# Kernel optimization log

Hardware: AMD Instinct MI355X
Metric: run time of the kernel (lower is better)

The kernel has to match this reference:

```python
import jax, jax.numpy as jnp
import numpy as np

M, N, P, T = 8000, 63, 64, 5


def setup_inputs() -> dict:
    key = jax.random.key(0)
    ks = jax.random.split(key, 19)
    sn = (1.0 / N) ** 0.5
    sp = (1.0 / P) ** 0.5
    f32 = jnp.float32
    return {
        "A": jax.random.normal(ks[0], (1, M, N), f32),
        "b": jax.random.normal(ks[1], (1, M), f32),
        "c": jax.random.normal(ks[2], (1, N), f32),
        "theta1r": sn * jax.random.normal(ks[3], (P, N + 1), f32),
        "theta1c": sn * jax.random.normal(ks[4], (P, N + 1), f32),
        "theta2rr": sp * jax.random.normal(ks[5], (P, P), f32),
        "theta2rc": sp * jax.random.normal(ks[6], (P, P), f32),
        "theta2cr": sp * jax.random.normal(ks[7], (P, P), f32),
        "theta3rr": sp * jax.random.normal(ks[8], (P, P), f32),
        "theta3rc": sp * jax.random.normal(ks[9], (P, P), f32),
        "theta3cr": sp * jax.random.normal(ks[10], (P, P), f32),
        "theta4rr": sp * jax.random.normal(ks[11], (P,), f32),
        "theta4rc": sp * jax.random.normal(ks[12], (P,), f32),
        "theta4cr": sp * jax.random.normal(ks[13], (P,), f32),
        "theta6r": sp * jax.random.normal(ks[14], (P, P), f32),
        "theta6c": sp * jax.random.normal(ks[15], (P, P), f32),
        "theta7": sp * jax.random.normal(ks[16], (P, P), f32),
        "W8": 0.05 * jax.random.normal(ks[17], (2, 2 * P), f32),
        "b8": 0.05 * jax.random.normal(ks[18], (2,), f32),
        "z": 7,
    }


def reference(A, b, c, theta1r, theta1c, theta2rr, theta2rc, theta2cr,
              theta3rr, theta3rc, theta3cr, theta4rr, theta4rc, theta4cr,
              theta6r, theta6c, theta7, W8, b8, z):
    relu = jax.nn.relu
    m, n = A.shape[1], A.shape[2]
    p = theta1r.shape[0]
    # raw node features: row node v -> [A[v,:], b[v]]; column node m -> [c, 0]
    Fr_raw = jnp.concatenate([A[0], b[0][:, None]], axis=1)        # (m, n+1)
    fc_raw = jnp.concatenate([c[0], jnp.zeros((1,), A.dtype)])     # (n+1,)
    Fr = Fr_raw / jnp.linalg.norm(Fr_raw, axis=1, keepdims=True)   # f(v), v < m
    fc = fc_raw / jnp.linalg.norm(fc_raw)                          # f(m)
    # edge weights w(v,u) = f(v).f(u) are detached in the original (float(...data))
    Frd = jax.lax.stop_gradient(Fr)
    fcd = jax.lax.stop_gradient(fc)
    Wrr = Frd @ Frd.T                                              # (m, m)
    dg = jnp.diagonal(Wrr)
    srr_pos = relu(Wrr).sum(axis=1) - relu(dg)                     # sum over u != v
    srr_neg = relu(-Wrr).sum(axis=1) - relu(-dg)
    wrc = Frd @ fcd                                                # (m,) = w(v, m)
    # identity: sum_u relu(t4 * w_u) = relu(t4) * sum_u relu(w_u) + relu(-t4) * sum_u relu(-w_u)
    Srr = relu(theta4rr)[:, None] * srr_pos[None, :] + relu(-theta4rr)[:, None] * srr_neg[None, :]
    Src = relu(theta4rc)[:, None] * relu(wrc)[None, :] + relu(-theta4rc)[:, None] * relu(-wrc)[None, :]
    scr = relu(theta4cr) * relu(wrc).sum() + relu(-theta4cr) * relu(-wrc).sum()
    edge_r = theta3rr @ Srr + theta3rc @ Src                       # (p, m), constant over t
    edge_c = theta3cr @ scr                                        # (p,)
    fz = Fr[z]                                                     # z < m: row node feature
    t1r = theta1r @ fz                                             # (p,)
    t1c = theta1c @ fz
    # mu init (p, m+1) = [[Ab^T, c0^T]; 0]; split into row columns / column node
    mu_r0 = jnp.zeros((p, m), A.dtype).at[: n + 1].set(Fr_raw.T)
    mu_c0 = jnp.zeros((p,), A.dtype).at[: n + 1].set(fc_raw)

    def step(carry, _):
        mu_r, mu_c = carry
        # row nodes: term2rr uses old mu[:, v]; term2rc uses old mu[:, m]
        new_r = relu(t1r[:, None] + theta2rr @ mu_r + (theta2rc @ mu_c)[:, None] + edge_r)
        # column node updated last within a sweep -> sees updated row embeddings
        new_c = relu(t1c + theta2cr @ new_r.sum(axis=1) + edge_c)
        return (new_r, new_c), None

    (mu_r, mu_c), _ = jax.lax.scan(step, (mu_r0, mu_c0), None, length=T)
    term6 = theta6r @ mu_r.sum(axis=1) + theta6c @ mu_c            # (p,)
    term7 = theta7 @ mu_r[:, z]                                    # (p,)
    feat = jax.nn.sigmoid(jnp.concatenate([term6, term7]))         # (2p,)
    return (feat @ W8.T + b8)[None, :]                             # (1, 2)
```

## Files before the change

kernel.cpp:

```cpp
#include <hip/hip_runtime.h>
#include <math.h>

typedef __attribute__((ext_vector_type(8))) short short8;
typedef __attribute__((ext_vector_type(4))) float f32x4;

#define WS_SPART 0
#define WS_GPART 262144
#define WS_WPART 270336
#define WS_CPART 270592
#define WS_T1R   310592
#define WS_T1C   310656
#define WS_AL    310720
#define WS_BE    310784
#define WS_GA    310848
#define WS_DE    310912
#define WS_ECP   310976
#define WS_ECN   311040
#define WS_W     311104
#define WS_MUZ   311168
#define WS_WSUM  311232
#define WS_RNORM 311296
#define WS_R2H   319488
#define WS_R2L   321536
#define WS_E4    323584
#define WS_FH    355584
#define WS_FL    617728

__device__ __forceinline__ float waveReduceSum(float v) {
#pragma unroll
    for (int m = 32; m >= 1; m >>= 1) v += __shfl_xor(v, m, 64);
    return v;
}
__device__ __forceinline__ unsigned short f2bf(float f) {
    unsigned int u = __float_as_uint(f);
    unsigned int r = (u + 0x7fffu + ((u >> 16) & 1u)) >> 16;
    return (unsigned short)r;
}
__device__ __forceinline__ float bf2f(unsigned short h) {
    return __uint_as_float(((unsigned int)h) << 16);
}

__global__ __launch_bounds__(256) void k_fr(
    const float* __restrict__ A, const float* __restrict__ b, const float* __restrict__ c,
    const float* __restrict__ th1r, const float* __restrict__ th1c,
    const float* __restrict__ th2rr, const float* __restrict__ th2rc,
    const float* __restrict__ th3rr, const float* __restrict__ th3rc, const float* __restrict__ th3cr,
    const float* __restrict__ th4rr, const float* __restrict__ th4rc, const float* __restrict__ th4cr,
    const int* __restrict__ zp,
    unsigned short* __restrict__ Fh, unsigned short* __restrict__ Fl,
    unsigned short* __restrict__ R2H, unsigned short* __restrict__ R2L,
    float* __restrict__ ws)
{
    int tid = threadIdx.x, lane = tid & 63, wid = tid >> 6;

    if (blockIdx.x == 128) {
        __shared__ float fcraw[64], fz[64], sh4a[64], sh4b[64];
        int p = lane;
        int z = zp[0];
        float cv = (p < 63) ? c[p] : 0.f;
        fcraw[p] = cv;
        float av = (p < 63) ? A[z * 63 + p] : b[z];
        float s2 = waveReduceSum(av * av);
        fz[p] = av * rsqrtf(s2);
        __syncthreads();

        float t1 = 0.f, t2 = 0.f, w0 = 0.f;
#pragma unroll 8
        for (int k = 0; k < 64; k++) {
            t1 += th1r[p * 64 + k] * fz[k];
            t2 += th1c[p * 64 + k] * fz[k];
            w0 += th2rc[p * 64 + k] * fcraw[k];
        }
        ws[WS_T1R + p] = t1;
        ws[WS_T1C + p] = t2;
        ws[WS_W + p] = t1 + w0;

        sh4a[p] = th4rr[p];
        sh4b[p] = th4rc[p];
        __syncthreads();
        float a = 0.f, bb = 0.f, g = 0.f, d = 0.f;
#pragma unroll 8
        for (int k = 0; k < 64; k++) {
            float t4 = sh4a[k];
            a  += th3rr[p * 64 + k] * fmaxf(t4, 0.f);
            bb += th3rr[p * 64 + k] * fmaxf(-t4, 0.f);
            float t5 = sh4b[k];
            g  += th3rc[p * 64 + k] * fmaxf(t5, 0.f);
            d  += th3rc[p * 64 + k] * fmaxf(-t5, 0.f);
        }
        ws[WS_AL + p] = a; ws[WS_BE + p] = bb;
        ws[WS_GA + p] = g; ws[WS_DE + p] = d;
        __syncthreads();
        sh4a[p] = th4cr[p];
        __syncthreads();
        float e1 = 0.f, e2 = 0.f;
#pragma unroll 8
        for (int k = 0; k < 64; k++) {
            float t6 = sh4a[k];
            e1 += th3cr[p * 64 + k] * fmaxf(t6, 0.f);
            e2 += th3cr[p * 64 + k] * fmaxf(-t6, 0.f);
        }
        ws[WS_ECP + p] = e1; ws[WS_ECN + p] = e2;

#pragma unroll
        for (int i = 0; i < 16; i++) {
            int idx = tid * 16 + i;
            float f = th2rr[idx];
            unsigned short h = f2bf(f);
            R2H[idx] = h;
            R2L[idx] = f2bf(f - bf2f(h));
        }
        return;
    }

    __shared__ float gsh[64];
    __shared__ float wsh2[2];
    if (tid < 64) gsh[tid] = 0.f;
    if (tid < 2) wsh2[tid] = 0.f;
    __syncthreads();

    float cv = (lane < 63) ? c[lane] : 0.f;
    float cn2 = waveReduceSum(cv * cv);
    float fcnl = cv * rsqrtf(cn2);

    int gw = blockIdx.x * 4 + wid;
    float gl = 0.f, lp = 0.f, ln = 0.f;
    for (int r = gw; r < 8192; r += 512) {
        if (r < 8000) {
            float val = (lane < 63) ? A[r * 63 + lane] : b[r];
            float s2 = waveReduceSum(val * val);
            float f = val * rsqrtf(s2);
            unsigned short h = f2bf(f);
            Fh[r * 64 + lane] = h;
            Fl[r * 64 + lane] = f2bf(f - bf2f(h));
            gl += f;
            float w = waveReduceSum(f * fcnl);
            if (lane == 0) {
                ws[WS_RNORM + r] = sqrtf(s2);
                lp += fmaxf(w, 0.f); ln += fmaxf(-w, 0.f);
            }
        } else {
            Fh[r * 64 + lane] = 0;
            Fl[r * 64 + lane] = 0;
        }
    }
    atomicAdd(&gsh[lane], gl);
    if (lane == 0) { atomicAdd(&wsh2[0], lp); atomicAdd(&wsh2[1], ln); }
    __syncthreads();
    if (tid < 64) ws[WS_GPART + blockIdx.x * 64 + tid] = gsh[tid];
    if (tid == 64) ws[WS_WPART + blockIdx.x * 2 + 0] = wsh2[0];
    if (tid == 65) ws[WS_WPART + blockIdx.x * 2 + 1] = wsh2[1];
}

__global__ __launch_bounds__(256) void k_gram(
    const unsigned short* __restrict__ Fh, const unsigned short* __restrict__ Fl,
    float* __restrict__ ws)
{
    int tid = threadIdx.x, lane = tid & 63, wid = tid >> 6;
    int m = lane & 15, quad = lane >> 4;
    int vbase = blockIdx.x * 256 + wid * 64;

    short8 AH[8], AL[8];
#pragma unroll
    for (int pt = 0; pt < 4; pt++)
#pragma unroll
        for (int q = 0; q < 2; q++) {
            int off = (vbase + pt * 16 + m) * 64 + q * 32 + quad * 8;
            AH[pt * 2 + q] = *(const short8*)(Fh + off);
            AL[pt * 2 + q] = *(const short8*)(Fl + off);
        }
    float srr[16];
#pragma unroll
    for (int i = 0; i < 16; i++) srr[i] = 0.f;

    const int y = blockIdx.y;
    const int boff = m * 64 + quad * 8;
    short8 B0h[2], B0l[2], B1h[2], B1l[2];
#pragma unroll
    for (int q = 0; q < 2; q++) {
        B0h[q] = *(const short8*)(Fh + y * 16 * 64 + boff + q * 32);
        B0l[q] = *(const short8*)(Fl + y * 16 * 64 + boff + q * 32);
    }
#pragma unroll 1
    for (int ii = 0; ii < 8; ii++) {
        int tB1 = y + 64 * ii + 32;
#pragma unroll
        for (int q = 0; q < 2; q++) {
            B1h[q] = *(const short8*)(Fh + tB1 * 16 * 64 + boff + q * 32);
            B1l[q] = *(const short8*)(Fl + tB1 * 16 * 64 + boff + q * 32);
        }
#pragma unroll
        for (int pt = 0; pt < 4; pt++) {
            f32x4 a = {0.f, 0.f, 0.f, 0.f};
#pragma unroll
            for (int q = 0; q < 2; q++) {
                a = __builtin_amdgcn_mfma_f32_16x16x32_bf16(AH[pt*2+q], B0h[q], a, 0, 0, 0);
                a = __builtin_amdgcn_mfma_f32_16x16x32_bf16(AH[pt*2+q], B0l[q], a, 0, 0, 0);
                a = __builtin_amdgcn_mfma_f32_16x16x32_bf16(AL[pt*2+q], B0h[q], a, 0, 0, 0);
            }
#pragma unroll
            for (int r = 0; r < 4; r++) srr[pt*4+r] += fmaxf(a[r], 0.f);
        }
        if (ii < 7) {
            int tB0 = y + 64 * ii + 64;
#pragma unroll
            for (int q = 0; q < 2; q++) {
                B0h[q] = *(const short8*)(Fh + tB0 * 16 * 64 + boff + q * 32);
                B0l[q] = *(const short8*)(Fl + tB0 * 16 * 64 + boff + q * 32);
            }
        }
#pragma unroll
        for (int pt = 0; pt < 4; pt++) {
            f32x4 a = {0.f, 0.f, 0.f, 0.f};
#pragma unroll
            for (int q = 0; q < 2; q++) {
                a = __builtin_amdgcn_mfma_f32_16x16x32_bf16(AH[pt*2+q], B1h[q], a, 0, 0, 0);
                a = __builtin_amdgcn_mfma_f32_16x16x32_bf16(AH[pt*2+q], B1l[q], a, 0, 0, 0);
                a = __builtin_amdgcn_mfma_f32_16x16x32_bf16(AL[pt*2+q], B1h[q], a, 0, 0, 0);
            }
#pragma unroll
            for (int r = 0; r < 4; r++) srr[pt*4+r] += fmaxf(a[r], 0.f);
        }
    }
#pragma unroll
    for (int pt = 0; pt < 4; pt++)
#pragma unroll
        for (int r = 0; r < 4; r++) {
            float s = srr[pt * 4 + r];
#pragma unroll
            for (int mm = 8; mm >= 1; mm >>= 1) s += __shfl_xor(s, mm, 64);
            if (m == 0)
                ws[WS_SPART + y * 8192 + vbase + pt * 16 + quad * 4 + r] = s;
        }
}

__global__ __launch_bounds__(256) void k_e4(
    const float* __restrict__ c, float* __restrict__ ws,
    unsigned short* __restrict__ MH, unsigned short* __restrict__ ML)
{
    __shared__ float fcnS[64], gS[64], sprow[64], red[256];
    int tid = threadIdx.x, lane = tid & 63, wid = tid >> 6;

    float cv = (lane < 63) ? c[lane] : 0.f;
    float cn2 = waveReduceSum(cv * cv);
    if (wid == 0) fcnS[lane] = cv * rsqrtf(cn2);

    float gv = 0.f;
#pragma unroll 8
    for (int blk = wid * 32; blk < wid * 32 + 32; blk++)
        gv += ws[WS_GPART + blk * 64 + lane];
    red[tid] = gv;
    __syncthreads();
    if (tid < 64) gS[tid] = red[tid] + red[64 + tid] + red[128 + tid] + red[192 + tid];
    if (wid == 1) {
        float wp = ws[WS_WPART + lane * 2] + ws[WS_WPART + (lane + 64) * 2];
        wp = waveReduceSum(wp);
        if (lane == 0) ws[WS_WSUM] = wp;
    }
    if (wid == 2) {
        float wn = ws[WS_WPART + lane * 2 + 1] + ws[WS_WPART + (lane + 64) * 2 + 1];
        wn = waveReduceSum(wn);
        if (lane == 0) ws[WS_WSUM + 1] = wn;
    }
    int v0 = blockIdx.x * 64;
    float sv = 0.f;
#pragma unroll
    for (int y = wid * 8; y < wid * 8 + 8; y++)
        sv += ws[WS_SPART + y * 8192 + v0 + lane];
    __syncthreads();
    red[tid] = sv;
    __syncthreads();
    if (tid < 64) sprow[tid] = red[tid] + red[64 + tid] + red[128 + tid] + red[192 + tid];
    __syncthreads();

    for (int i2 = 0; i2 < 16; i2++) {
        int i = wid * 16 + i2;
        int v = v0 + i;
        unsigned short fh = MH[v * 64 + lane];
        unsigned short fl = ML[v * 64 + lane];
        float fr = bf2f(fh) + bf2f(fl);
        float dw = waveReduceSum(fr * fcnS[lane]);
        float dg = waveReduceSum(fr * gS[lane]);
        if (lane == 0) {
            float spv = sprow[i];
            float4 e;
            e.x = spv - 1.0f;
            e.y = spv - dg;
            e.z = fmaxf(dw, 0.f);
            e.w = fmaxf(-dw, 0.f);
            *(float4*)(ws + WS_E4 + v * 4) = e;
        }
        float rnv = ws[WS_RNORM + v];
        float x = fr * rnv;
        unsigned short h = f2bf(x);
        MH[v * 64 + lane] = h;
        ML[v * 64 + lane] = f2bf(x - bf2f(h));
    }
}

__global__ __launch_bounds__(256) void k_iter(
    const float* __restrict__ th2cr, const float* __restrict__ th2rc,
    const int* __restrict__ zp, float* __restrict__ ws,
    unsigned short* __restrict__ MH, unsigned short* __restrict__ ML,
    const unsigned short* __restrict__ R2H, const unsigned short* __restrict__ R2L,
    int t)
{
    __shared__ __align__(16) float wsh[64], alS[64], beS[64], gaS[64], deS[64];
    __shared__ float red[256], Ssh[64], ysh[64], colp[256];
    int tid = threadIdx.x, lane = tid & 63, wid = tid >> 6;
    int m = lane & 15, quad = lane >> 4;
    int v = (blockIdx.x * 4 + wid) * 16 + m;

    if (tid < 64) {
        alS[tid] = ws[WS_AL + tid]; beS[tid] = ws[WS_BE + tid];
        gaS[tid] = ws[WS_GA + tid]; deS[tid] = ws[WS_DE + tid];
    }
    if (t == 0) {
        if (tid >= 64 && tid < 128) wsh[tid - 64] = ws[WS_W + tid - 64];
        __syncthreads();
    } else {
        float s = 0.f;
        for (int blk = wid; blk < 125; blk += 4)
            s += ws[WS_CPART + (t - 1) * 8000 + blk * 64 + lane];
        red[tid] = s;
        __syncthreads();
        if (tid < 64) Ssh[tid] = red[tid] + red[64 + tid] + red[128 + tid] + red[192 + tid];
        __syncthreads();
        {
            int p = wid * 16 + m;
            float acc = 0.f;
            const float4* rowp = (const float4*)(th2cr + p * 64 + quad * 16);
#pragma unroll
            for (int kk = 0; kk < 4; kk++) {
                float4 r4 = rowp[kk];
                acc += r4.x * Ssh[quad * 16 + 4 * kk]     + r4.y * Ssh[quad * 16 + 4 * kk + 1]
                     + r4.z * Ssh[quad * 16 + 4 * kk + 2] + r4.w * Ssh[quad * 16 + 4 * kk + 3];
            }
            acc += __shfl_xor(acc, 16, 64);
            acc += __shfl_xor(acc, 32, 64);
            if (quad == 0)
                ysh[p] = fmaxf(acc + ws[WS_T1C + p] + ws[WS_WSUM] * ws[WS_ECP + p]
                               + ws[WS_WSUM + 1] * ws[WS_ECN + p], 0.f);
        }
        __syncthreads();
        {
            int p = wid * 16 + m;
            float acc = 0.f;
            const float4* rowp = (const float4*)(th2rc + p * 64 + quad * 16);
#pragma unroll
            for (int kk = 0; kk < 4; kk++) {
                float4 r4 = rowp[kk];
                acc += r4.x * ysh[quad * 16 + 4 * kk]     + r4.y * ysh[quad * 16 + 4 * kk + 1]
                     + r4.z * ysh[quad * 16 + 4 * kk + 2] + r4.w * ysh[quad * 16 + 4 * kk + 3];
            }
            acc += __shfl_xor(acc, 16, 64);
            acc += __shfl_xor(acc, 32, 64);
            if (quad == 0) wsh[p] = acc + ws[WS_T1R + p];
        }
        __syncthreads();
    }

    short8 RH[8], RL[8];
#pragma unroll
    for (int pt = 0; pt < 4; pt++)
#pragma unroll
        for (int q = 0; q < 2; q++) {
            int off = (pt * 16 + m) * 64 + q * 32 + quad * 8;
            RH[pt * 2 + q] = *(const short8*)(R2H + off);
            RL[pt * 2 + q] = *(const short8*)(R2L + off);
        }
    short8 BH[2], BL[2];
#pragma unroll
    for (int q = 0; q < 2; q++) {
        BH[q] = *(const short8*)(MH + v * 64 + q * 32 + quad * 8);
        BL[q] = *(const short8*)(ML + v * 64 + q * 32 + quad * 8);
    }
    float4 e = *(const float4*)(ws + WS_E4 + v * 4);
    int z = zp[0];

#pragma unroll
    for (int pt = 0; pt < 4; pt++) {
        f32x4 a = {0.f, 0.f, 0.f, 0.f};
#pragma unroll
        for (int q = 0; q < 2; q++) {
            a = __builtin_amdgcn_mfma_f32_16x16x32_bf16(RH[pt*2+q], BH[q], a, 0, 0, 0);
            a = __builtin_amdgcn_mfma_f32_16x16x32_bf16(RH[pt*2+q], BL[q], a, 0, 0, 0);
            a = __builtin_amdgcn_mfma_f32_16x16x32_bf16(RL[pt*2+q], BH[q], a, 0, 0, 0);
        }
        int pbase = pt * 16 + quad * 4;
        float4 w4 = *(const float4*)(wsh + pbase);
        float4 a4 = *(const float4*)(alS + pbase);
        float4 b4 = *(const float4*)(beS + pbase);
        float4 g4 = *(const float4*)(gaS + pbase);
        float4 d4 = *(const float4*)(deS + pbase);
        float v0 = fmaxf(a[0] + w4.x + a4.x*e.x + b4.x*e.y + g4.x*e.z + d4.x*e.w, 0.f);
        float v1 = fmaxf(a[1] + w4.y + a4.y*e.x + b4.y*e.y + g4.y*e.z + d4.y*e.w, 0.f);
        float v2 = fmaxf(a[2] + w4.z + a4.z*e.x + b4.z*e.y + g4.z*e.z + d4.z*e.w, 0.f);
        float v3 = fmaxf(a[3] + w4.w + a4.w*e.x + b4.w*e.y + g4.w*e.z + d4.w*e.w, 0.f);
        ushort4 h4, l4;
        h4.x = f2bf(v0); l4.x = f2bf(v0 - bf2f(h4.x));
        h4.y = f2bf(v1); l4.y = f2bf(v1 - bf2f(h4.y));
        h4.z = f2bf(v2); l4.z = f2bf(v2 - bf2f(h4.z));
        h4.w = f2bf(v3); l4.w = f2bf(v3 - bf2f(h4.w));
        *(ushort4*)(MH + v * 64 + pbase) = h4;
        *(ushort4*)(ML + v * 64 + pbase) = l4;
        float c0 = v0, c1 = v1, c2 = v2, c3 = v3;
#pragma unroll
        for (int mm = 1; mm < 16; mm <<= 1) {
            c0 += __shfl_xor(c0, mm, 64);
            c1 += __shfl_xor(c1, mm, 64);
            c2 += __shfl_xor(c2, mm, 64);
            c3 += __shfl_xor(c3, mm, 64);
        }
        if (m == 0) {
            colp[wid * 64 + pbase + 0] = c0;
            colp[wid * 64 + pbase + 1] = c1;
            colp[wid * 64 + pbase + 2] = c2;
            colp[wid * 64 + pbase + 3] = c3;
        }
        if (t == 4 && v == z) {
            float4 o; o.x = v0; o.y = v1; o.z = v2; o.w = v3;
            *(float4*)(ws + WS_MUZ + pbase) = o;
        }
    }
    __syncthreads();
    if (tid < 64)
        ws[WS_CPART + t * 8000 + blockIdx.x * 64 + tid] =
            colp[tid] + colp[64 + tid] + colp[128 + tid] + colp[192 + tid];
}

__global__ __launch_bounds__(256) void k_head(
    const float* __restrict__ th2cr,
    const float* __restrict__ th6r, const float* __restrict__ th6c, const float* __restrict__ th7,
    const float* __restrict__ W8, const float* __restrict__ b8,
    float* __restrict__ ws, float* __restrict__ out)
{
    int tid = threadIdx.x, lane = tid & 63, wid = tid >> 6;
    __shared__ float red[256], S[64], y[64], feat[128];
    float s = 0.f;
    for (int blk = wid; blk < 125; blk += 4)
        s += ws[WS_CPART + 4 * 8000 + blk * 64 + lane];
    red[tid] = s;
    __syncthreads();
    if (tid < 64) S[tid] = red[tid] + red[64 + tid] + red[128 + tid] + red[192 + tid];
    __syncthreads();
    int p = tid;
    if (p < 64) {
        float acc = ws[WS_T1C + p] + ws[WS_WSUM] * ws[WS_ECP + p]
                  + ws[WS_WSUM + 1] * ws[WS_ECN + p];
#pragma unroll 8
        for (int k = 0; k < 64; k++) acc += th2cr[p * 64 + k] * S[k];
        y[p] = fmaxf(acc, 0.f);
    }
    __syncthreads();
    if (p < 64) {
        float t6 = 0.f, t7 = 0.f;
#pragma unroll 8
        for (int k = 0; k < 64; k++) {
            t6 += th6r[p * 64 + k] * S[k] + th6c[p * 64 + k] * y[k];
            t7 += th7[p * 64 + k] * ws[WS_MUZ + k];
        }
        feat[p] = 1.f / (1.f + expf(-t6));
        feat[64 + p] = 1.f / (1.f + expf(-t7));
    }
    __syncthreads();
    if (p < 2) {
        float o = b8[p];
        for (int i = 0; i < 128; i++) o += W8[p * 128 + i] * feat[i];
        out[p] = o;
    }
}

extern "C" void kernel_launch(void* const* d_in, const int* in_sizes, int n_in,
                              void* d_out, int out_size, void* d_ws, size_t ws_size,
                              hipStream_t stream) {
    (void)in_sizes; (void)n_in; (void)out_size; (void)ws_size;
    const float* A     = (const float*)d_in[0];
    const float* b     = (const float*)d_in[1];
    const float* c     = (const float*)d_in[2];
    const float* th1r  = (const float*)d_in[3];
    const float* th1c  = (const float*)d_in[4];
    const float* th2rr = (const float*)d_in[5];
    const float* th2rc = (const float*)d_in[6];
    const float* th2cr = (const float*)d_in[7];
    const float* th3rr = (const float*)d_in[8];
    const float* th3rc = (const float*)d_in[9];
    const float* th3cr = (const float*)d_in[10];
    const float* th4rr = (const float*)d_in[11];
    const float* th4rc = (const float*)d_in[12];
    const float* th4cr = (const float*)d_in[13];
    const float* th6r  = (const float*)d_in[14];
    const float* th6c  = (const float*)d_in[15];
    const float* th7   = (const float*)d_in[16];
    const float* W8    = (const float*)d_in[17];
    const float* b8    = (const float*)d_in[18];
    const int*   zp    = (const int*)d_in[19];
    float* ws  = (float*)d_ws;
    float* out = (float*)d_out;
    unsigned short* Fh  = (unsigned short*)(ws + WS_FH);
    unsigned short* Fl  = (unsigned short*)(ws + WS_FL);
    unsigned short* R2H = (unsigned short*)(ws + WS_R2H);
    unsigned short* R2L = (unsigned short*)(ws + WS_R2L);

    k_fr<<<129, 256, 0, stream>>>(A, b, c, th1r, th1c, th2rr, th2rc, th3rr, th3rc,
                                  th3cr, th4rr, th4rc, th4cr, zp, Fh, Fl, R2H, R2L, ws);
    k_gram<<<dim3(32, 32), 256, 0, stream>>>(Fh, Fl, ws);
    k_e4<<<125, 256, 0, stream>>>(c, ws, Fh, Fl);
    for (int t = 0; t < 5; t++)
        k_iter<<<125, 256, 0, stream>>>(th2cr, th2rc, zp, ws, Fh, Fl, R2H, R2L, t);
    k_head<<<1, 256, 0, stream>>>(th2cr, th6r, th6c, th7, W8, b8, ws, out);
}
```

Before: 238.1 us.

## Stage Gram B tiles in LDS, widen row-norm grid, split iteration into mu and column kernels

Measured after the change: 239.0 us. No clear change (+0.4%).

```diff
diff --git a/kernel.cpp b/kernel.cpp
--- a/kernel.cpp
+++ b/kernel.cpp
@@ -5,26 +5,26 @@
 typedef __attribute__((ext_vector_type(4))) float f32x4;
 
 #define WS_SPART 0
-#define WS_GPART 262144
-#define WS_WPART 270336
-#define WS_CPART 270592
-#define WS_T1R   310592
-#define WS_T1C   310656
-#define WS_AL    310720
-#define WS_BE    310784
-#define WS_GA    310848
-#define WS_DE    310912
-#define WS_ECP   310976
-#define WS_ECN   311040
-#define WS_W     311104
-#define WS_MUZ   311168
-#define WS_WSUM  311232
-#define WS_RNORM 311296
-#define WS_R2H   319488
-#define WS_R2L   321536
-#define WS_E4    323584
-#define WS_FH    355584
-#define WS_FL    617728
+#define WS_GPART 131072
+#define WS_WPART 163840
+#define WS_CPART 164864
+#define WS_T1R   204864
+#define WS_T1C   204928
+#define WS_AL    204992
+#define WS_BE    205056
+#define WS_GA    205120
+#define WS_DE    205184
+#define WS_ECP   205248
+#define WS_ECN   205312
+#define WS_W     205376
+#define WS_MUZ   205760
+#define WS_WSUM  205824
+#define WS_RNORM 205888
+#define WS_R2H   214080
+#define WS_R2L   216128
+#define WS_E4    218176
+#define WS_FH    250176
+#define WS_FL    512320
 
 __device__ __forceinline__ float waveReduceSum(float v) {
 #pragma unroll
@@ -53,7 +53,7 @@
 {
     int tid = threadIdx.x, lane = tid & 63, wid = tid >> 6;
 
-    if (blockIdx.x == 128) {
+    if (blockIdx.x == 512) {
         __shared__ float fcraw[64], fz[64], sh4a[64], sh4b[64];
         int p = lane;
         int z = zp[0];
@@ -123,9 +123,11 @@
     float cn2 = waveReduceSum(cv * cv);
     float fcnl = cv * rsqrtf(cn2);
 
-    int gw = blockIdx.x * 4 + wid;
+    int r0 = blockIdx.x * 16 + wid * 4;
     float gl = 0.f, lp = 0.f, ln = 0.f;
-    for (int r = gw; r < 8192; r += 512) {
+#pragma unroll
+    for (int i = 0; i < 4; i++) {
+        int r = r0 + i;
         if (r < 8000) {
             float val = (lane < 63) ? A[r * 63 + lane] : b[r];
             float s2 = waveReduceSum(val * val);
@@ -156,9 +158,12 @@
     const unsigned short* __restrict__ Fh, const unsigned short* __restrict__ Fl,
     float* __restrict__ ws)
 {
+    __shared__ short BshH[2][16 * 72];
+    __shared__ short BshL[2][16 * 72];
     int tid = threadIdx.x, lane = tid & 63, wid = tid >> 6;
     int m = lane & 15, quad = lane >> 4;
     int vbase = blockIdx.x * 256 + wid * 64;
+    int sr = tid >> 4, sc = (tid & 15) * 4;
 
     short8 AH[8], AL[8];
 #pragma unroll
@@ -174,52 +179,44 @@
     for (int i = 0; i < 16; i++) srr[i] = 0.f;
 
     const int y = blockIdx.y;
-    const int boff = m * 64 + quad * 8;
-    short8 B0h[2], B0l[2], B1h[2], B1l[2];
-#pragma unroll
-    for (int q = 0; q < 2; q++) {
-        B0h[q] = *(const short8*)(Fh + y * 16 * 64 + boff + q * 32);
-        B0l[q] = *(const short8*)(Fl + y * 16 * 64 + boff + q * 32);
-    }
+    {
+        int u0 = y * 16;
+        *(uint2*)(&BshH[0][sr * 72 + sc]) = *(const uint2*)(Fh + (u0 + sr) * 64 + sc);
+        *(uint2*)(&BshL[0][sr * 72 + sc]) = *(const uint2*)(Fl + (u0 + sr) * 64 + sc);
+    }
+    __syncthreads();
+
 #pragma unroll 1
-    for (int ii = 0; ii < 8; ii++) {
-        int tB1 = y + 64 * ii + 32;
+    for (int k = 0; k < 32; k++) {
+        int cur = k & 1;
+        uint2 sH, sL;
+        if (k < 31) {
+            int u0 = (y + 16 * (k + 1)) * 16;
+            sH = *(const uint2*)(Fh + (u0 + sr) * 64 + sc);
+            sL = *(const uint2*)(Fl + (u0 + sr) * 64 + sc);
+        }
+        short8 BH[2], BL[2];
 #pragma unroll
         for (int q = 0; q < 2; q++) {
-            B1h[q] = *(const short8*)(Fh + tB1 * 16 * 64 + boff + q * 32);
-            B1l[q] = *(const short8*)(Fl + tB1 * 16 * 64 + boff + q * 32);
+            BH[q] = *(const short8*)(&BshH[cur][m * 72 + q * 32 + quad * 8]);
+            BL[q] = *(const short8*)(&BshL[cur][m * 72 + q * 32 + quad * 8]);
         }
 #pragma unroll
         for (int pt = 0; pt < 4; pt++) {
             f32x4 a = {0.f, 0.f, 0.f, 0.f};
 #pragma unroll
             for (int q = 0; q < 2; q++) {
-                a = __builtin_amdgcn_mfma_f32_16x16x32_bf16(AH[pt*2+q], B0h[q], a, 0, 0, 0);
-                a = __builtin_amdgcn_mfma_f32_16x16x32_bf16(AH[pt*2+q], B0l[q], a, 0, 0, 0);
-                a = __builtin_amdgcn_mfma_f32_16x16x32_bf16(AL[pt*2+q], B0h[q], a, 0, 0, 0);
+                a = __builtin_amdgcn_mfma_f32_16x16x32_bf16(AH[pt*2+q], BH[q], a, 0, 0, 0);
+                a = __builtin_amdgcn_mfma_f32_16x16x32_bf16(AH[pt*2+q], BL[q], a, 0, 0, 0);
+                a = __builtin_amdgcn_mfma_f32_16x16x32_bf16(AL[pt*2+q], BH[q], a, 0, 0, 0);
             }
 #pragma unroll
             for (int r = 0; r < 4; r++) srr[pt*4+r] += fmaxf(a[r], 0.f);
         }
-        if (ii < 7) {
-            int tB0 = y + 64 * ii + 64;
-#pragma unroll
-            for (int q = 0; q < 2; q++) {
-                B0h[q] = *(const short8*)(Fh + tB0 * 16 * 64 + boff + q * 32);
-                B0l[q] = *(const short8*)(Fl + tB0 * 16 * 64 + boff + q * 32);
-            }
-        }
-#pragma unroll
-        for (int pt = 0; pt < 4; pt++) {
-            f32x4 a = {0.f, 0.f, 0.f, 0.f};
-#pragma unroll
-            for (int q = 0; q < 2; q++) {
-                a = __builtin_amdgcn_mfma_f32_16x16x32_bf16(AH[pt*2+q], B1h[q], a, 0, 0, 0);
-                a = __builtin_amdgcn_mfma_f32_16x16x32_bf16(AH[pt*2+q], B1l[q], a, 0, 0, 0);
-                a = __builtin_amdgcn_mfma_f32_16x16x32_bf16(AL[pt*2+q], B1h[q], a, 0, 0, 0);
-            }
-#pragma unroll
-            for (int r = 0; r < 4; r++) srr[pt*4+r] += fmaxf(a[r], 0.f);
+        if (k < 31) {
+            *(uint2*)(&BshH[1 - cur][sr * 72 + sc]) = sH;
+            *(uint2*)(&BshL[1 - cur][sr * 72 + sc]) = sL;
+            __syncthreads();
         }
     }
 #pragma unroll
@@ -246,27 +243,28 @@
     if (wid == 0) fcnS[lane] = cv * rsqrtf(cn2);
 
     float gv = 0.f;
-#pragma unroll 8
-    for (int blk = wid * 32; blk < wid * 32 + 32; blk++)
-        gv += ws[WS_GPART + blk * 64 + lane];
+    for (int bb = 0; bb < 128; bb++) gv += ws[WS_GPART + (wid * 128 + bb) * 64 + lane];
     red[tid] = gv;
     __syncthreads();
     if (tid < 64) gS[tid] = red[tid] + red[64 + tid] + red[128 + tid] + red[192 + tid];
     if (wid == 1) {
-        float wp = ws[WS_WPART + lane * 2] + ws[WS_WPART + (lane + 64) * 2];
+        float wp = 0.f;
+#pragma unroll
+        for (int k = 0; k < 8; k++) wp += ws[WS_WPART + (lane + 64 * k) * 2];
         wp = waveReduceSum(wp);
         if (lane == 0) ws[WS_WSUM] = wp;
     }
     if (wid == 2) {
-        float wn = ws[WS_WPART + lane * 2 + 1] + ws[WS_WPART + (lane + 64) * 2 + 1];
+        float wn = 0.f;
+#pragma unroll
+        for (int k = 0; k < 8; k++) wn += ws[WS_WPART + (lane + 64 * k) * 2 + 1];
         wn = waveReduceSum(wn);
         if (lane == 0) ws[WS_WSUM + 1] = wn;
     }
     int v0 = blockIdx.x * 64;
     float sv = 0.f;
 #pragma unroll
-    for (int y = wid * 8; y < wid * 8 + 8; y++)
-        sv += ws[WS_SPART + y * 8192 + v0 + lane];
+    for (int y = wid * 4; y < wid * 4 + 4; y++) sv += ws[WS_SPART + y * 8192 + v0 + lane];
     __syncthreads();
     red[tid] = sv;
     __syncthreads();
@@ -276,9 +274,7 @@
     for (int i2 = 0; i2 < 16; i2++) {
         int i = wid * 16 + i2;
         int v = v0 + i;
-        unsigned short fh = MH[v * 64 + lane];
-        unsigned short fl = ML[v * 64 + lane];
-        float fr = bf2f(fh) + bf2f(fl);
+        float fr = bf2f(MH[v * 64 + lane]) + bf2f(ML[v * 64 + lane]);
         float dw = waveReduceSum(fr * fcnS[lane]);
         float dg = waveReduceSum(fr * gS[lane]);
         if (lane == 0) {
@@ -290,75 +286,29 @@
             e.w = fmaxf(-dw, 0.f);
             *(float4*)(ws + WS_E4 + v * 4) = e;
         }
-        float rnv = ws[WS_RNORM + v];
-        float x = fr * rnv;
+        float x = fr * ws[WS_RNORM + v];
         unsigned short h = f2bf(x);
         MH[v * 64 + lane] = h;
         ML[v * 64 + lane] = f2bf(x - bf2f(h));
     }
 }
 
-__global__ __launch_bounds__(256) void k_iter(
-    const float* __restrict__ th2cr, const float* __restrict__ th2rc,
+__global__ __launch_bounds__(256) void k_mu(
     const int* __restrict__ zp, float* __restrict__ ws,
     unsigned short* __restrict__ MH, unsigned short* __restrict__ ML,
     const unsigned short* __restrict__ R2H, const unsigned short* __restrict__ R2L,
     int t)
 {
-    __shared__ __align__(16) float wsh[64], alS[64], beS[64], gaS[64], deS[64];
-    __shared__ float red[256], Ssh[64], ysh[64], colp[256];
+    __shared__ __align__(16) float wS[64], alS[64], beS[64], gaS[64], deS[64];
+    __shared__ float colp[256];
     int tid = threadIdx.x, lane = tid & 63, wid = tid >> 6;
     int m = lane & 15, quad = lane >> 4;
     int v = (blockIdx.x * 4 + wid) * 16 + m;
-
-    if (tid < 64) {
-        alS[tid] = ws[WS_AL + tid]; beS[tid] = ws[WS_BE + tid];
-        gaS[tid] = ws[WS_GA + tid]; deS[tid] = ws[WS_DE + tid];
-    }
-    if (t == 0) {
-        if (tid >= 64 && tid < 128) wsh[tid - 64] = ws[WS_W + tid - 64];
-        __syncthreads();
-    } else {
-        float s = 0.f;
-        for (int blk = wid; blk < 125; blk += 4)
-            s += ws[WS_CPART + (t - 1) * 8000 + blk * 64 + lane];
-        red[tid] = s;
-        __syncthreads();
-        if (tid < 64) Ssh[tid] = red[tid] + red[64 + tid] + red[128 + tid] + red[192 + tid];
-        __syncthreads();
-        {
-            int p = wid * 16 + m;
-            float acc = 0.f;
-            const float4* rowp = (const float4*)(th2cr + p * 64 + quad * 16);
-#pragma unroll
-            for (int kk = 0; kk < 4; kk++) {
-                float4 r4 = rowp[kk];
-                acc += r4.x * Ssh[quad * 16 + 4 * kk]     + r4.y * Ssh[quad * 16 + 4 * kk + 1]
-                     + r4.z * Ssh[quad * 16 + 4 * kk + 2] + r4.w * Ssh[quad * 16 + 4 * kk + 3];
-            }
-            acc += __shfl_xor(acc, 16, 64);
-            acc += __shfl_xor(acc, 32, 64);
-            if (quad == 0)
-                ysh[p] = fmaxf(acc + ws[WS_T1C + p] + ws[WS_WSUM] * ws[WS_ECP + p]
-                               + ws[WS_WSUM + 1] * ws[WS_ECN + p], 0.f);
-        }
-        __syncthreads();
-        {
-            int p = wid * 16 + m;
-            float acc = 0.f;
-            const float4* rowp = (const float4*)(th2rc + p * 64 + quad * 16);
-#pragma unroll
-            for (int kk = 0; kk < 4; kk++) {
-                float4 r4 = rowp[kk];
-                acc += r4.x * ysh[quad * 16 + 4 * kk]     + r4.y * ysh[quad * 16 + 4 * kk + 1]
-                     + r4.z * ysh[quad * 16 + 4 * kk + 2] + r4.w * ysh[quad * 16 + 4 * kk + 3];
-            }
-            acc += __shfl_xor(acc, 16, 64);
-            acc += __shfl_xor(acc, 32, 64);
-            if (quad == 0) wsh[p] = acc + ws[WS_T1R + p];
-        }
-        __syncthreads();
-    }
+    int z = zp[0];
+
+    if (wid == 0) wS[lane] = ws[WS_W + t * 64 + lane];
+    else if (wid == 1) { alS[lane] = ws[WS_AL + lane]; beS[lane] = ws[WS_BE + lane]; }
+    else if (wid == 2) { gaS[lane] = ws[WS_GA + lane]; deS[lane] = ws[WS_DE + lane]; }
 
     short8 RH[8], RL[8];
 #pragma unroll
@@ -376,7 +326,7 @@
         BL[q] = *(const short8*)(ML + v * 64 + q * 32 + quad * 8);
     }
     float4 e = *(const float4*)(ws + WS_E4 + v * 4);
-    int z = zp[0];
+    __syncthreads();
 
 #pragma unroll
     for (int pt = 0; pt < 4; pt++) {
@@ -388,23 +338,23 @@
             a = __builtin_amdgcn_mfma_f32_16x16x32_bf16(RL[pt*2+q], BH[q], a, 0, 0, 0);
         }
         int pbase = pt * 16 + quad * 4;
-        float4 w4 = *(const float4*)(wsh + pbase);
+        float4 w4 = *(const float4*)(wS + pbase);
         float4 a4 = *(const float4*)(alS + pbase);
         float4 b4 = *(const float4*)(beS + pbase);
         float4 g4 = *(const float4*)(gaS + pbase);
         float4 d4 = *(const float4*)(deS + pbase);
-        float v0 = fmaxf(a[0] + w4.x + a4.x*e.x + b4.x*e.y + g4.x*e.z + d4.x*e.w, 0.f);
-        float v1 = fmaxf(a[1] + w4.y + a4.y*e.x + b4.y*e.y + g4.y*e.z + d4.y*e.w, 0.f);
-        float v2 = fmaxf(a[2] + w4.z + a4.z*e.x + b4.z*e.y + g4.z*e.z + d4.z*e.w, 0.f);
-        float v3 = fmaxf(a[3] + w4.w + a4.w*e.x + b4.w*e.y + g4.w*e.z + d4.w*e.w, 0.f);
+        float u0 = fmaxf(a[0] + w4.x + a4.x*e.x + b4.x*e.y + g4.x*e.z + d4.x*e.w, 0.f);
+        float u1 = fmaxf(a[1] + w4.y + a4.y*e.x + b4.y*e.y + g4.y*e.z + d4.y*e.w, 0.f);
+        float u2 = fmaxf(a[2] + w4.z + a4.z*e.x + b4.z*e.y + g4.z*e.z + d4.z*e.w, 0.f);
+        float u3 = fmaxf(a[3] + w4.w + a4.w*e.x + b4.w*e.y + g4.w*e.z + d4.w*e.w, 0.f);
         ushort4 h4, l4;
-        h4.x = f2bf(v0); l4.x = f2bf(v0 - bf2f(h4.x));
-        h4.y = f2bf(v1); l4.y = f2bf(v1 - bf2f(h4.y));
-        h4.z = f2bf(v2); l4.z = f2bf(v2 - bf2f(h4.z));
-        h4.w = f2bf(v3); l4.w = f2bf(v3 - bf2f(h4.w));
+        h4.x = f2bf(u0); l4.x = f2bf(u0 - bf2f(h4.x));
+        h4.y = f2bf(u1); l4.y = f2bf(u1 - bf2f(h4.y));
+        h4.z = f2bf(u2); l4.z = f2bf(u2 - bf2f(h4.z));
+        h4.w = f2bf(u3); l4.w = f2bf(u3 - bf2f(h4.w));
         *(ushort4*)(MH + v * 64 + pbase) = h4;
         *(ushort4*)(ML + v * 64 + pbase) = l4;
-        float c0 = v0, c1 = v1, c2 = v2, c3 = v3;
+        float c0 = u0, c1 = u1, c2 = u2, c3 = u3;
 #pragma unroll
         for (int mm = 1; mm < 16; mm <<= 1) {
             c0 += __shfl_xor(c0, mm, 64);
@@ -419,7 +369,7 @@
             colp[wid * 64 + pbase + 3] = c3;
         }
         if (t == 4 && v == z) {
-            float4 o; o.x = v0; o.y = v1; o.z = v2; o.w = v3;
+            float4 o; o.x = u0; o.y = u1; o.z = u2; o.w = u3;
             *(float4*)(ws + WS_MUZ + pbase) = o;
         }
     }
@@ -429,45 +379,76 @@
             colp[tid] + colp[64 + tid] + colp[128 + tid] + colp[192 + tid];
 }
 
-__global__ __launch_bounds__(256) void k_head(
-    const float* __restrict__ th2cr,
-    const float* __restrict__ th6r, const float* __restrict__ th6c, const float* __restrict__ th7,
-    const float* __restrict__ W8, const float* __restrict__ b8,
-    float* __restrict__ ws, float* __restrict__ out)
+__global__ __launch_bounds__(256) void k_colup(
+    const float* __restrict__ th2cr, const float* __restrict__ th2rc,
+    const float* __restrict__ th6r, const float* __restrict__ th6c,
+    const float* __restrict__ th7, const float* __restrict__ W8,
+    const float* __restrict__ b8,
+    float* __restrict__ ws, float* __restrict__ out, int t)
 {
+    __shared__ float red[256], Ssh[64], ysh[64], wsh[64], feat[128];
     int tid = threadIdx.x, lane = tid & 63, wid = tid >> 6;
-    __shared__ float red[256], S[64], y[64], feat[128];
+    int m = lane & 15, quad = lane >> 4;
+
     float s = 0.f;
     for (int blk = wid; blk < 125; blk += 4)
-        s += ws[WS_CPART + 4 * 8000 + blk * 64 + lane];
+        s += ws[WS_CPART + t * 8000 + blk * 64 + lane];
     red[tid] = s;
     __syncthreads();
-    if (tid < 64) S[tid] = red[tid] + red[64 + tid] + red[128 + tid] + red[192 + tid];
-    __syncthreads();
-    int p = tid;
-    if (p < 64) {
-        float acc = ws[WS_T1C + p] + ws[WS_WSUM] * ws[WS_ECP + p]
-                  + ws[WS_WSUM + 1] * ws[WS_ECN + p];
+    if (tid < 64) Ssh[tid] = red[tid] + red[64 + tid] + red[128 + tid] + red[192 + tid];
+    __syncthreads();
+    {
+        int p = wid * 16 + m;
+        float acc = 0.f;
+        const float4* rowp = (const float4*)(th2cr + p * 64 + quad * 16);
+#pragma unroll
+        for (int kk = 0; kk < 4; kk++) {
+            float4 r4 = rowp[kk];
+            acc += r4.x * Ssh[quad * 16 + 4 * kk]     + r4.y * Ssh[quad * 16 + 4 * kk + 1]
+                 + r4.z * Ssh[quad * 16 + 4 * kk + 2] + r4.w * Ssh[quad * 16 + 4 * kk + 3];
+        }
+        acc += __shfl_xor(acc, 16, 64);
+        acc += __shfl_xor(acc, 32, 64);
+        if (quad == 0)
+            ysh[p] = fmaxf(acc + ws[WS_T1C + p] + ws[WS_WSUM] * ws[WS_ECP + p]
+                           + ws[WS_WSUM + 1] * ws[WS_ECN + p], 0.f);
+    }
+    __syncthreads();
+    {
+        int p = wid * 16 + m;
+        float acc = 0.f;
+        const float4* rowp = (const float4*)(th2rc + p * 64 + quad * 16);
+#pragma unroll
+        for (int kk = 0; kk < 4; kk++) {
+            float4 r4 = rowp[kk];
+            acc += r4.x * ysh[quad * 16 + 4 * kk]     + r4.y * ysh[quad * 16 + 4 * kk + 1]
+                 + r4.z * ysh[quad * 16 + 4 * kk + 2] + r4.w * ysh[quad * 16 + 4 * kk + 3];
+        }
+        acc += __shfl_xor(acc, 16, 64);
+        acc += __shfl_xor(acc, 32, 64);
+        if (quad == 0) wsh[p] = acc + ws[WS_T1R + p];
+    }
+    __syncthreads();
+    if (tid < 64) ws[WS_W + (t + 1) * 64 + tid] = wsh[tid];
+
+    if (t == 4) {
+        int p = tid;
+        if (p < 64) {
+            float t6 = 0.f, t7 = 0.f;
 #pragma unroll 8
-        for (int k = 0; k < 64; k++) acc += th2cr[p * 64 + k] * S[k];
-        y[p] = fmaxf(acc, 0.f);
-    }
-    __syncthreads();
-    if (p < 64) {
-        float t6 = 0.f, t7 = 0.f;
-#pragma unroll 8
-        for (int k = 0; k < 64; k++) {
-            t6 += th6r[p * 64 + k] * S[k] + th6c[p * 64 + k] * y[k];
-            t7 += th7[p * 64 + k] * ws[WS_MUZ + k];
-        }
-        feat[p] = 1.f / (1.f + expf(-t6));
-        feat[64 + p] = 1.f / (1.f + expf(-t7));
-    }
-    __syncthreads();
-    if (p < 2) {
-        float o = b8[p];
-        for (int i = 0; i < 128; i++) o += W8[p * 128 + i] * feat[i];
-        out[p] = o;
+            for (int k = 0; k < 64; k++) {
+                t6 += th6r[p * 64 + k] * Ssh[k] + th6c[p * 64 + k] * ysh[k];
+                t7 += th7[p * 64 + k] * ws[WS_MUZ + k];
+            }
+            feat[p] = 1.f / (1.f + expf(-t6));
+            feat[64 + p] = 1.f / (1.f + expf(-t7));
+        }
+        __syncthreads();
+        if (p < 2) {
+            float o = b8[p];
+            for (int i = 0; i < 128; i++) o += W8[p * 128 + i] * feat[i];
+            out[p] = o;
+        }
     }
 }
 
@@ -502,11 +483,12 @@
     unsigned short* R2H = (unsigned short*)(ws + WS_R2H);
     unsigned short* R2L = (unsigned short*)(ws + WS_R2L);
 
-    k_fr<<<129, 256, 0, stream>>>(A, b, c, th1r, th1c, th2rr, th2rc, th3rr, th3rc,
+    k_fr<<<513, 256, 0, stream>>>(A, b, c, th1r, th1c, th2rr, th2rc, th3rr, th3rc,
                                   th3cr, th4rr, th4rc, th4cr, zp, Fh, Fl, R2H, R2L, ws);
-    k_gram<<<dim3(32, 32), 256, 0, stream>>>(Fh, Fl, ws);
+    k_gram<<<dim3(32, 16), 256, 0, stream>>>(Fh, Fl, ws);
     k_e4<<<125, 256, 0, stream>>>(c, ws, Fh, Fl);
-    for (int t = 0; t < 5; t++)
-        k_iter<<<125, 256, 0, stream>>>(th2cr, th2rc, zp, ws, Fh, Fl, R2H, R2L, t);
-    k_head<<<1, 256, 0, stream>>>(th2cr, th6r, th6c, th7, W8, b8, ws, out);
-}
+    for (int t = 0; t < 5; t++) {
+        k_mu<<<125, 256, 0, stream>>>(zp, ws, Fh, Fl, R2H, R2L, t);
+        k_colup<<<1, 256, 0, stream>>>(th2cr, th2rc, th6r, th6c, th7, W8, b8, ws, out, t);
+    }
+}
```
